# Performance work log

Measured on AMD Instinct MI355X. Metric: run time of the kernel, lower is better.

The kernel has to match this reference:

```python
import jax, jax.numpy as jnp
import numpy as np

DIM = 1024
HEADS = 16
DIM_HEAD = 64
INNER = HEADS * DIM_HEAD  # 1024
SCALE = DIM_HEAD ** -0.5


def setup_inputs() -> dict:
    key = jax.random.key(0)
    k_x, k_qkv, k_out, k_g, k_b = jax.random.split(key, 5)
    x = jax.random.normal(k_x, (4, 2048, DIM), dtype=jnp.float32)
    # LayerNorm affine params (torch default: weight=1, bias=0; keep learnable-shaped)
    ln_gamma = jnp.ones((DIM,), dtype=jnp.float32)
    ln_beta = jnp.zeros((DIM,), dtype=jnp.float32)
    w_qkv = jax.random.normal(k_qkv, (DIM, 3 * INNER), dtype=jnp.float32) * (DIM ** -0.5)
    w_out = jax.random.normal(k_out, (INNER, DIM), dtype=jnp.float32) * (INNER ** -0.5)
    return {"x": x, "ln_gamma": ln_gamma, "ln_beta": ln_beta, "w_qkv": w_qkv, "w_out": w_out}


def reference(x, ln_gamma, ln_beta, w_qkv, w_out):
    # LayerNorm (eps matches torch default 1e-5)
    mu = jnp.mean(x, axis=-1, keepdims=True)
    var = jnp.mean(jnp.square(x - mu), axis=-1, keepdims=True)
    xn = (x - mu) * jax.lax.rsqrt(var + 1e-5) * ln_gamma + ln_beta

    qkv = xn @ w_qkv  # [b, n, 3*inner]
    q, k, v = jnp.split(qkv, 3, axis=-1)

    def to_heads(t):  # b n (h d) -> b h n d
        b, n, _ = t.shape
        return t.reshape(b, n, HEADS, DIM_HEAD).transpose(0, 2, 1, 3)

    q, k, v = to_heads(q), to_heads(k), to_heads(v)

    dots = jnp.einsum('bhid,bhjd->bhij', q, k) * SCALE  # [b,h,n,n]
    attn = jax.nn.softmax(dots, axis=-1)
    out = jnp.einsum('bhij,bhjd->bhid', attn, v)  # [b,h,n,d]

    b, h, n, d = out.shape
    out = out.transpose(0, 2, 1, 3).reshape(b, n, h * d)  # b h n d -> b n (h d)
    return out @ w_out
```

## Files before the change

kernel.cpp:

```cpp
#include <hip/hip_runtime.h>

#define DIM 1024
#define HEADS 16
#define DHEAD 64
#define SEQ 2048
#define BATCH 4
#define ROWS (BATCH*SEQ)
#define QK_COLS (3*DIM)
#define QSCALE 0.18033688011112042f

typedef __bf16 bf16x8 __attribute__((ext_vector_type(8)));
typedef __bf16 bf16x4 __attribute__((ext_vector_type(4)));
typedef short s16x4 __attribute__((ext_vector_type(4)));
typedef float f32x4 __attribute__((ext_vector_type(4)));
typedef unsigned short u16;
typedef unsigned int u32;

__device__ __forceinline__ u16 f2bf(float f) {
  u32 u = __float_as_uint(f);
  u = (u + 0x7fffu + ((u >> 16) & 1u)) >> 16;
  return (u16)u;
}

__device__ __forceinline__ void gld16(const void* g, void* s) {
  __builtin_amdgcn_global_load_lds((__attribute__((address_space(1))) void*)g,
                                   (__attribute__((address_space(3))) void*)s, 16, 0, 0);
}

__device__ __forceinline__ float fexp2(float x) {
#if defined(__HIP_DEVICE_COMPILE__)
  return __builtin_amdgcn_exp2f(x);
#else
  return x;
#endif
}

__device__ __forceinline__ s16x4 pack_bf16(f32x4 v) {
  bf16x4 b = __builtin_convertvector(v, bf16x4);
  union { bf16x4 b; s16x4 s; } u; u.b = b; return u.s;
}

__global__ __launch_bounds__(256) void prep_kernel(
    const float* __restrict__ x, const float* __restrict__ gam, const float* __restrict__ bet,
    u16* __restrict__ xn,
    const float* __restrict__ wqkv, u16* __restrict__ wqkvT,
    const float* __restrict__ wout, u16* __restrict__ woutT) {
  __shared__ float tile[32][33];
  int bid = blockIdx.x, tid = threadIdx.x;
  if (bid < ROWS) {
    int lane = tid & 63, w = tid >> 6;
    const float4 xv = *(const float4*)(x + (size_t)bid*DIM + tid*4);
    float s = xv.x + xv.y + xv.z + xv.w;
    float q = xv.x*xv.x + xv.y*xv.y + xv.z*xv.z + xv.w*xv.w;
    for (int off = 32; off > 0; off >>= 1) { s += __shfl_xor(s, off, 64); q += __shfl_xor(q, off, 64); }
    float* red = &tile[0][0];
    if (lane == 0) { red[w] = s; red[4+w] = q; }
    __syncthreads();
    s = red[0]+red[1]+red[2]+red[3];
    q = red[4]+red[5]+red[6]+red[7];
    float mean = s * (1.0f/DIM);
    float rstd = rsqrtf(q*(1.0f/DIM) - mean*mean + 1e-5f);
    float4 gv = *(const float4*)(gam + tid*4);
    float4 bv = *(const float4*)(bet + tid*4);
    ushort4 o;
    o.x = f2bf((xv.x-mean)*rstd*gv.x + bv.x);
    o.y = f2bf((xv.y-mean)*rstd*gv.y + bv.y);
    o.z = f2bf((xv.z-mean)*rstd*gv.z + bv.z);
    o.w = f2bf((xv.w-mean)*rstd*gv.w + bv.w);
    *(ushort4*)(xn + (size_t)bid*DIM + tid*4) = o;
  } else {
    const float* in; u16* out; int R, C, c0, r0;
    if (bid < ROWS + 3072) {
      int t = bid - ROWS;
      in = wqkv; out = wqkvT; R = DIM; C = QK_COLS;
      c0 = (t % 96) * 32; r0 = (t / 96) * 32;
    } else {
      int t = bid - ROWS - 3072;
      in = wout; out = woutT; R = DIM; C = DIM;
      c0 = (t & 31) * 32; r0 = (t >> 5) * 32;
    }
    int tx = tid & 31, ty = tid >> 5;
    for (int i = 0; i < 32; i += 8)
      tile[ty+i][tx] = in[(size_t)(r0+ty+i)*C + c0 + tx];
    __syncthreads();
    for (int i = 0; i < 32; i += 8)
      out[(size_t)(c0+ty+i)*R + r0 + tx] = f2bf(tile[tx][ty+i]);
  }
}

template<int NOUT, int EPI>
__global__ __launch_bounds__(256, 2) void gemm_bt(const u16* __restrict__ A, const u16* __restrict__ Bt,
                                                  void* __restrict__ Cv, u16* __restrict__ vT, int K) {
  __shared__ alignas(16) u16 smem[16384];
  int tid = threadIdx.x;
  int lane = tid & 63, w = tid >> 6;
  int l = lane & 15, quad = lane >> 4;
  int wm = (w & 1) * 64, wn = (w >> 1) * 64;
  int m0 = blockIdx.y * 128, n0 = blockIdx.x * 128;
  const u16* Ag = A + (size_t)m0 * K;
  const u16* Bg = Bt + (size_t)n0 * K;
  bool sw = (EPI == 1) || (n0 < 2048);
  f32x4 z = {0.f, 0.f, 0.f, 0.f};
  f32x4 acc[4][4];
  for (int i = 0; i < 4; ++i) for (int j = 0; j < 4; ++j) acc[i][j] = z;

  #pragma unroll
  for (int c = 0; c < 2; ++c) {
    int idx = c*256 + tid;
    int row = idx >> 2, col = (idx & 3) << 3;
    gld16(Ag + (size_t)row*K + col, smem + idx*8);
    gld16(Bg + (size_t)row*K + col, smem + 4096 + idx*8);
  }

  int NT = K >> 5;
  for (int kt = 0; kt < NT; ++kt) {
    __syncthreads();
    const u16* As = smem + (kt & 1)*8192;
    const u16* Bs = As + 4096;
    if (kt + 1 < NT) {
      u16* dst = (u16*)smem + ((kt+1) & 1)*8192;
      int ko = (kt+1)*32;
      #pragma unroll
      for (int c = 0; c < 2; ++c) {
        int idx = c*256 + tid;
        int row = idx >> 2, col = (idx & 3) << 3;
        gld16(Ag + (size_t)row*K + ko + col, dst + idx*8);
        gld16(Bg + (size_t)row*K + ko + col, dst + 4096 + idx*8);
      }
    }
    bf16x8 af[4], bfr[4];
    #pragma unroll
    for (int t = 0; t < 4; ++t) {
      af[t]  = *(const bf16x8*)(As + (wm + t*16 + l)*32 + quad*8);
      bfr[t] = *(const bf16x8*)(Bs + (wn + t*16 + l)*32 + quad*8);
    }
    if (sw) {
      #pragma unroll
      for (int i = 0; i < 4; ++i)
        #pragma unroll
        for (int j = 0; j < 4; ++j)
          acc[i][j] = __builtin_amdgcn_mfma_f32_16x16x32_bf16(bfr[i], af[j], acc[i][j], 0, 0, 0);
    } else {
      #pragma unroll
      for (int i = 0; i < 4; ++i)
        #pragma unroll
        for (int j = 0; j < 4; ++j)
          acc[i][j] = __builtin_amdgcn_mfma_f32_16x16x32_bf16(af[i], bfr[j], acc[i][j], 0, 0, 0);
    }
  }

  if (EPI == 0) {
    u16* C = (u16*)Cv;
    int region = n0 >> 10;
    if (region == 0) {
      for (int i = 0; i < 4; ++i)
        for (int j = 0; j < 4; ++j) {
          int nq = n0 + wn + i*16 + quad*4;
          int m  = m0 + wm + j*16 + l;
          f32x4 v = acc[i][j] * QSCALE;
          *(s16x4*)(C + (size_t)m*QK_COLS + nq) = pack_bf16(v);
        }
    } else if (region == 1) {
      for (int i = 0; i < 4; ++i)
        for (int j = 0; j < 4; ++j) {
          int nq = n0 + wn + i*16 + quad*4;
          int m  = m0 + wm + j*16 + l;
          int d  = nq & 63;
          int col = (nq & ~63) | ((((d >> 3) ^ (m & 7)) << 3) | (d & 7));
          *(s16x4*)(C + (size_t)m*QK_COLS + col) = pack_bf16(acc[i][j]);
        }
    } else {
      for (int i = 0; i < 4; ++i)
        for (int j = 0; j < 4; ++j) {
          int mrow = m0 + wm + i*16 + quad*4;
          int hd   = (n0 - 2048) + wn + j*16 + l;
          int h = hd >> 6, d = hd & 63;
          int bb = mrow >> 11, nloc = mrow & 2047;
          int jloc = nloc & 31;
          int hi = jloc >> 4;
          int u  = ((nloc >> 5) & 3) * 4 + ((jloc >> 2) & 3);
          int c16 = u ^ (d & 15);
          int p = (nloc & ~127) | (c16 << 3) | (hi << 2);
          *(s16x4*)(vT + ((size_t)(bb*16 + h)*DHEAD + d)*SEQ + p) = pack_bf16(acc[i][j]);
        }
    }
  } else {
    float* C = (float*)Cv;
    for (int i = 0; i < 4; ++i)
      for (int j = 0; j < 4; ++j) {
        int n = n0 + wn + i*16 + quad*4;
        int m = m0 + wm + j*16 + l;
        *(f32x4*)(C + (size_t)m*NOUT + n) = acc[i][j];
      }
  }
}

__global__ __launch_bounds__(256, 2) void attn_kernel(const u16* __restrict__ qkv,
    const u16* __restrict__ vT, u16* __restrict__ aout) {
  __shared__ alignas(16) u16 smem[32768];
  int tid = threadIdx.x;
  int lane = tid & 63, w = tid >> 6;
  int l = lane & 15, quad = lane >> 4;
  int bh = blockIdx.x, qt = blockIdx.y;
  int b = bh >> 4, h = bh & 15;
  int qrow0 = b*SEQ + qt*128;

  bf16x8 aq[2][2];
  #pragma unroll
  for (int mt = 0; mt < 2; ++mt)
    #pragma unroll
    for (int ks = 0; ks < 2; ++ks)
      aq[mt][ks] = *(const bf16x8*)(qkv + (size_t)(qrow0 + w*32 + mt*16 + l)*QK_COLS + h*DHEAD + ks*32 + quad*8);

  f32x4 z = {0.f,0.f,0.f,0.f};
  f32x4 o[4][2];
  #pragma unroll
  for (int dt = 0; dt < 4; ++dt) for (int mt = 0; mt < 2; ++mt) o[dt][mt] = z;
  f32x4 psum[2] = {z, z};

  const u16* kbase = qkv + (size_t)b*SEQ*QK_COLS + DIM + h*DHEAD;
  const u16* vbase = vT + (size_t)bh*DHEAD*SEQ;

  #pragma unroll
  for (int c = 0; c < 4; ++c) {
    int idx = c*256 + tid;
    gld16(kbase + (size_t)(idx >> 3)*QK_COLS + ((idx & 7) << 3), smem + idx*8);
    gld16(vbase + (size_t)(idx >> 4)*SEQ + ((idx & 15) << 3), smem + 8192 + idx*8);
  }

  for (int kt = 0; kt < 16; ++kt) {
    __syncthreads();
    const u16* Kt = smem + (kt & 1)*16384;
    const u16* Vt = Kt + 8192;
    if (kt < 15) {
      u16* dst = (u16*)smem + ((kt+1) & 1)*16384;
      int krow0 = (kt+1)*128;
      #pragma unroll
      for (int c = 0; c < 4; ++c) {
        int idx = c*256 + tid;
        gld16(kbase + (size_t)(krow0 + (idx >> 3))*QK_COLS + ((idx & 7) << 3), dst + idx*8);
        gld16(vbase + (size_t)(idx >> 4)*SEQ + krow0 + ((idx & 15) << 3), dst + 8192 + idx*8);
      }
    }

    s16x4 pb[2][8];
    #pragma unroll
    for (int mt = 0; mt < 2; ++mt) {
      f32x4 st[8];
      #pragma unroll
      for (int jt = 0; jt < 8; ++jt) st[jt] = z;
      #pragma unroll
      for (int jt = 0; jt < 8; ++jt) {
        #pragma unroll
        for (int ks = 0; ks < 2; ++ks) {
          bf16x8 bk = *(const bf16x8*)(Kt + (jt*16 + l)*64 + (((ks*4 + quad) ^ (l & 7)) << 3));
          st[jt] = __builtin_amdgcn_mfma_f32_16x16x32_bf16(bk, aq[mt][ks], st[jt], 0,0,0);
        }
      }
      #pragma unroll
      for (int jt = 0; jt < 8; ++jt) {
        f32x4 p;
        p[0] = fexp2(st[jt][0]); p[1] = fexp2(st[jt][1]);
        p[2] = fexp2(st[jt][2]); p[3] = fexp2(st[jt][3]);
        psum[mt] += p;
        pb[mt][jt] = pack_bf16(p);
      }
    }

    #pragma unroll
    for (int jb = 0; jb < 4; ++jb) {
      union { s16x4 h[2]; bf16x8 v; } p0, p1;
      p0.h[0] = pb[0][2*jb]; p0.h[1] = pb[0][2*jb+1];
      p1.h[0] = pb[1][2*jb]; p1.h[1] = pb[1][2*jb+1];
      #pragma unroll
      for (int dt = 0; dt < 4; ++dt) {
        int d = dt*16 + l;
        bf16x8 av = *(const bf16x8*)(Vt + d*128 + (((jb*4 + quad) ^ l) << 3));
        o[dt][0] = __builtin_amdgcn_mfma_f32_16x16x32_bf16(av, p0.v, o[dt][0], 0,0,0);
        o[dt][1] = __builtin_amdgcn_mfma_f32_16x16x32_bf16(av, p1.v, o[dt][1], 0,0,0);
      }
    }
  }

  float li[2];
  #pragma unroll
  for (int mt = 0; mt < 2; ++mt) {
    float ps = psum[mt][0] + psum[mt][1] + psum[mt][2] + psum[mt][3];
    ps += __shfl_xor(ps, 16, 64);
    ps += __shfl_xor(ps, 32, 64);
    li[mt] = ps;
  }

  __syncthreads();
  u16* Ep = smem + w*2304;
  #pragma unroll
  for (int mt = 0; mt < 2; ++mt) {
    float inv = 1.0f / li[mt];
    #pragma unroll
    for (int dt = 0; dt < 4; ++dt)
      #pragma unroll
      for (int r = 0; r < 4; ++r)
        Ep[(mt*16 + l)*72 + dt*16 + quad*4 + r] = f2bf(o[dt][mt][r] * inv);
  }
  __asm__ volatile("s_waitcnt lgkmcnt(0)" ::: "memory");
  int lr = lane >> 1, half = lane & 1;
  size_t grow = (size_t)qrow0 + w*32 + lr;
  #pragma unroll
  for (int k = 0; k < 4; ++k) {
    uint4 vv = *(const uint4*)(Ep + lr*72 + half*32 + k*8);
    *(uint4*)(aout + grow*DIM + h*DHEAD + half*32 + k*8) = vv;
  }
}

extern "C" void kernel_launch(void* const* d_in, const int* in_sizes, int n_in,
                              void* d_out, int out_size, void* d_ws, size_t ws_size,
                              hipStream_t stream) {
  const float* x    = (const float*)d_in[0];
  const float* gam  = (const float*)d_in[1];
  const float* bet  = (const float*)d_in[2];
  const float* wqkv = (const float*)d_in[3];
  const float* wout = (const float*)d_in[4];
  float* out = (float*)d_out;

  u16* xn    = (u16*)d_ws;
  u16* wqkvT = xn    + (size_t)ROWS*DIM;
  u16* woutT = wqkvT + (size_t)QK_COLS*DIM;
  u16* qkvb  = woutT + (size_t)DIM*DIM;
  u16* vTb   = qkvb  + (size_t)ROWS*QK_COLS;
  u16* aoutb = vTb   + (size_t)64*DHEAD*SEQ;

  prep_kernel<<<ROWS + 3072 + 1024, 256, 0, stream>>>(x, gam, bet, xn, wqkv, wqkvT, wout, woutT);
  gemm_bt<QK_COLS,0><<<dim3(QK_COLS/128, ROWS/128), 256, 0, stream>>>(xn, wqkvT, (void*)qkvb, vTb, DIM);
  attn_kernel<<<dim3(64, SEQ/128), 256, 0, stream>>>(qkvb, vTb, aoutb);
  gemm_bt<DIM,1><<<dim3(DIM/128, ROWS/128), 256, 0, stream>>>(aoutb, woutT, (void*)out, nullptr, DIM);
}
```

Before: 271.6 us.

## Replace 128x128 GEMM with 256x256 tiled, phase-pipelined GEMM using XCD-aware block remap

Replaces the 128x128, 256-thread GEMM with a 256x256-tile, 512-thread kernel used by both the QKV and output projections. The new kernel stages A and B in a multi-buffered 128KB LDS schedule split into eight phases, each with explicit barriers, s_setprio around the MFMA bursts and manual vmcnt waits. It also remaps block IDs across the 8 XCDs to improve L2 locality. Larger tiles raise arithmetic intensity and cut global reloads. In exchange, only 128 blocks cover the output projection, which can leave most CUs idle, and the LDS footprint limits occupancy to one block per CU.

```diff
diff --git a/kernel.cpp b/kernel.cpp
--- a/kernel.cpp
+++ b/kernel.cpp
@@ -88,92 +88,124 @@
   }
 }
 
-template<int NOUT, int EPI>
-__global__ __launch_bounds__(256, 2) void gemm_bt(const u16* __restrict__ A, const u16* __restrict__ Bt,
-                                                  void* __restrict__ Cv, u16* __restrict__ vT, int K) {
-  __shared__ alignas(16) u16 smem[16384];
+template<int EPI>
+__global__ __launch_bounds__(512, 2) void gemm256(const u16* __restrict__ A, const u16* __restrict__ Bt,
+                                                  void* __restrict__ Cv, u16* __restrict__ vT,
+                                                  int K, int NBN, int NOUT) {
+  __shared__ alignas(16) u16 smem[65536];
   int tid = threadIdx.x;
   int lane = tid & 63, w = tid >> 6;
   int l = lane & 15, quad = lane >> 4;
-  int wm = (w & 1) * 64, wn = (w >> 1) * 64;
-  int m0 = blockIdx.y * 128, n0 = blockIdx.x * 128;
+  int wr = w >> 2, wc = w & 3;
+  int nwg = gridDim.x;
+  int qq8 = nwg >> 3;
+  int wg = (blockIdx.x & 7) * qq8 + (blockIdx.x >> 3);
+  int bm = wg / NBN, bn = wg % NBN;
+  int m0 = bm * 256, n0 = bn * 256;
   const u16* Ag = A + (size_t)m0 * K;
   const u16* Bg = Bt + (size_t)n0 * K;
   bool sw = (EPI == 1) || (n0 < 2048);
   f32x4 z = {0.f, 0.f, 0.f, 0.f};
-  f32x4 acc[4][4];
-  for (int i = 0; i < 4; ++i) for (int j = 0; j < 4; ++j) acc[i][j] = z;
-
-  #pragma unroll
-  for (int c = 0; c < 2; ++c) {
-    int idx = c*256 + tid;
-    int row = idx >> 2, col = (idx & 3) << 3;
-    gld16(Ag + (size_t)row*K + col, smem + idx*8);
-    gld16(Bg + (size_t)row*K + col, smem + 4096 + idx*8);
-  }
-
-  int NT = K >> 5;
-  for (int kt = 0; kt < NT; ++kt) {
-    __syncthreads();
-    const u16* As = smem + (kt & 1)*8192;
-    const u16* Bs = As + 4096;
-    if (kt + 1 < NT) {
-      u16* dst = (u16*)smem + ((kt+1) & 1)*8192;
-      int ko = (kt+1)*32;
-      #pragma unroll
-      for (int c = 0; c < 2; ++c) {
-        int idx = c*256 + tid;
-        int row = idx >> 2, col = (idx & 3) << 3;
-        gld16(Ag + (size_t)row*K + ko + col, dst + idx*8);
-        gld16(Bg + (size_t)row*K + ko + col, dst + 4096 + idx*8);
-      }
-    }
-    bf16x8 af[4], bfr[4];
-    #pragma unroll
-    for (int t = 0; t < 4; ++t) {
-      af[t]  = *(const bf16x8*)(As + (wm + t*16 + l)*32 + quad*8);
-      bfr[t] = *(const bf16x8*)(Bs + (wn + t*16 + l)*32 + quad*8);
-    }
-    if (sw) {
-      #pragma unroll
-      for (int i = 0; i < 4; ++i)
-        #pragma unroll
-        for (int j = 0; j < 4; ++j)
-          acc[i][j] = __builtin_amdgcn_mfma_f32_16x16x32_bf16(bfr[i], af[j], acc[i][j], 0, 0, 0);
-    } else {
-      #pragma unroll
-      for (int i = 0; i < 4; ++i)
-        #pragma unroll
-        for (int j = 0; j < 4; ++j)
-          acc[i][j] = __builtin_amdgcn_mfma_f32_16x16x32_bf16(af[i], bfr[j], acc[i][j], 0, 0, 0);
-    }
+  f32x4 acc[32];
+  #pragma unroll
+  for (int i = 0; i < 32; ++i) acc[i] = z;
+
+  #define AOFF(d, ks) ((d)*32768 + (ks)*8192)
+  #define BOFF(d, ks) ((d)*32768 + 16384 + (ks)*8192)
+  #define STG(dstOff, srcG, kofs) do { \
+    _Pragma("unroll") \
+    for (int c_ = 0; c_ < 2; ++c_) { \
+      int ch_ = c_*512 + tid; \
+      gld16((srcG) + (size_t)(ch_ >> 2)*K + (kofs) + ((ch_ & 3) << 3), \
+            smem + (dstOff) + ch_*8); \
+    } } while (0)
+
+  #define PHASE(d, h, ks, STAGE, VMN) do { \
+    const u16* Ar_ = smem + AOFF(d, ks); \
+    const u16* Br_ = smem + BOFF(d, ks); \
+    bf16x8 af_[4], bf_[4]; \
+    _Pragma("unroll") \
+    for (int mi = 0; mi < 4; ++mi) \
+      af_[mi] = *(const bf16x8*)(Ar_ + (wr*128 + (h)*64 + mi*16 + l)*32 + quad*8); \
+    _Pragma("unroll") \
+    for (int ni = 0; ni < 4; ++ni) \
+      bf_[ni] = *(const bf16x8*)(Br_ + (wc*64 + ni*16 + l)*32 + quad*8); \
+    STAGE; \
+    __builtin_amdgcn_s_barrier(); \
+    __builtin_amdgcn_s_setprio(1); \
+    if (sw) { \
+      _Pragma("unroll") \
+      for (int ni = 0; ni < 4; ++ni) \
+        _Pragma("unroll") \
+        for (int mi = 0; mi < 4; ++mi) \
+          acc[ni*8 + (h)*4 + mi] = __builtin_amdgcn_mfma_f32_16x16x32_bf16(bf_[ni], af_[mi], acc[ni*8 + (h)*4 + mi], 0, 0, 0); \
+    } else { \
+      _Pragma("unroll") \
+      for (int mi = 0; mi < 4; ++mi) \
+        _Pragma("unroll") \
+        for (int ni = 0; ni < 4; ++ni) \
+          acc[((h)*4 + mi)*4 + ni] = __builtin_amdgcn_mfma_f32_16x16x32_bf16(af_[mi], bf_[ni], acc[((h)*4 + mi)*4 + ni], 0, 0, 0); \
+    } \
+    __builtin_amdgcn_s_setprio(0); \
+    VMN; \
+    __builtin_amdgcn_s_barrier(); \
+  } while (0)
+
+  STG(AOFF(0,0), Ag, 0);  STG(BOFF(0,0), Bg, 0);
+  STG(AOFF(0,1), Ag, 32); STG(BOFF(0,1), Bg, 32);
+  STG(AOFF(1,0), Ag, 64); STG(BOFF(1,0), Bg, 64);
+  __asm__ volatile("s_waitcnt vmcnt(4)" ::: "memory");
+  __builtin_amdgcn_s_barrier();
+
+  int NT2 = K >> 7;
+  for (int t = 0; t < NT2; ++t) {
+    bool nl = (t < NT2 - 1);
+    int k1 = (2*t + 1) * 64, k2 = (2*t + 2) * 64, k3 = (2*t + 3) * 64;
+    PHASE(0,0,0, { STG(AOFF(1,1), Ag, k1+32); }, {});
+    PHASE(0,1,0, { STG(BOFF(1,1), Bg, k1+32); }, {});
+    PHASE(0,0,1, { if (nl) STG(AOFF(0,0), Ag, k2); }, {});
+    PHASE(0,1,1, { if (nl) STG(BOFF(0,0), Bg, k2); },
+          { if (nl) __asm__ volatile("s_waitcnt vmcnt(4)" ::: "memory");
+            else    __asm__ volatile("s_waitcnt vmcnt(0)" ::: "memory"); });
+    PHASE(1,0,0, { if (nl) STG(AOFF(0,1), Ag, k2+32); }, {});
+    PHASE(1,1,0, { if (nl) STG(BOFF(0,1), Bg, k2+32); }, {});
+    PHASE(1,0,1, { if (nl) STG(AOFF(1,0), Ag, k3); }, {});
+    PHASE(1,1,1, { if (nl) STG(BOFF(1,0), Bg, k3); },
+          { if (nl) __asm__ volatile("s_waitcnt vmcnt(4)" ::: "memory");
+            else    __asm__ volatile("s_waitcnt vmcnt(0)" ::: "memory"); });
   }
 
   if (EPI == 0) {
     u16* C = (u16*)Cv;
     int region = n0 >> 10;
     if (region == 0) {
-      for (int i = 0; i < 4; ++i)
-        for (int j = 0; j < 4; ++j) {
-          int nq = n0 + wn + i*16 + quad*4;
-          int m  = m0 + wm + j*16 + l;
-          f32x4 v = acc[i][j] * QSCALE;
-          *(s16x4*)(C + (size_t)m*QK_COLS + nq) = pack_bf16(v);
+      #pragma unroll
+      for (int ni = 0; ni < 4; ++ni)
+        #pragma unroll
+        for (int mi = 0; mi < 8; ++mi) {
+          int n = n0 + wc*64 + ni*16 + quad*4;
+          int m = m0 + wr*128 + mi*16 + l;
+          f32x4 v = acc[ni*8 + mi] * QSCALE;
+          *(s16x4*)(C + (size_t)m*QK_COLS + n) = pack_bf16(v);
         }
     } else if (region == 1) {
-      for (int i = 0; i < 4; ++i)
-        for (int j = 0; j < 4; ++j) {
-          int nq = n0 + wn + i*16 + quad*4;
-          int m  = m0 + wm + j*16 + l;
+      #pragma unroll
+      for (int ni = 0; ni < 4; ++ni)
+        #pragma unroll
+        for (int mi = 0; mi < 8; ++mi) {
+          int nq = n0 + wc*64 + ni*16 + quad*4;
+          int m  = m0 + wr*128 + mi*16 + l;
           int d  = nq & 63;
           int col = (nq & ~63) | ((((d >> 3) ^ (m & 7)) << 3) | (d & 7));
-          *(s16x4*)(C + (size_t)m*QK_COLS + col) = pack_bf16(acc[i][j]);
+          *(s16x4*)(C + (size_t)m*QK_COLS + col) = pack_bf16(acc[ni*8 + mi]);
         }
     } else {
-      for (int i = 0; i < 4; ++i)
-        for (int j = 0; j < 4; ++j) {
-          int mrow = m0 + wm + i*16 + quad*4;
-          int hd   = (n0 - 2048) + wn + j*16 + l;
+      #pragma unroll
+      for (int mi = 0; mi < 8; ++mi)
+        #pragma unroll
+        for (int ni = 0; ni < 4; ++ni) {
+          int mrow = m0 + wr*128 + mi*16 + quad*4;
+          int hd   = (n0 - 2048) + wc*64 + ni*16 + l;
           int h = hd >> 6, d = hd & 63;
           int bb = mrow >> 11, nloc = mrow & 2047;
           int jloc = nloc & 31;
@@ -181,18 +213,24 @@
           int u  = ((nloc >> 5) & 3) * 4 + ((jloc >> 2) & 3);
           int c16 = u ^ (d & 15);
           int p = (nloc & ~127) | (c16 << 3) | (hi << 2);
-          *(s16x4*)(vT + ((size_t)(bb*16 + h)*DHEAD + d)*SEQ + p) = pack_bf16(acc[i][j]);
+          *(s16x4*)(vT + ((size_t)(bb*16 + h)*DHEAD + d)*SEQ + p) = pack_bf16(acc[mi*4 + ni]);
         }
     }
   } else {
     float* C = (float*)Cv;
-    for (int i = 0; i < 4; ++i)
-      for (int j = 0; j < 4; ++j) {
-        int n = n0 + wn + i*16 + quad*4;
-        int m = m0 + wm + j*16 + l;
-        *(f32x4*)(C + (size_t)m*NOUT + n) = acc[i][j];
-      }
-  }
+    #pragma unroll
+    for (int ni = 0; ni < 4; ++ni)
+      #pragma unroll
+      for (int mi = 0; mi < 8; ++mi) {
+        int n = n0 + wc*64 + ni*16 + quad*4;
+        int m = m0 + wr*128 + mi*16 + l;
+        *(f32x4*)(C + (size_t)m*NOUT + n) = acc[ni*8 + mi];
+      }
+  }
+  #undef PHASE
+  #undef STG
+  #undef AOFF
+  #undef BOFF
 }
 
 __global__ __launch_bounds__(256, 2) void attn_kernel(const u16* __restrict__ qkv,
@@ -330,7 +368,7 @@
   u16* aoutb = vTb   + (size_t)64*DHEAD*SEQ;
 
   prep_kernel<<<ROWS + 3072 + 1024, 256, 0, stream>>>(x, gam, bet, xn, wqkv, wqkvT, wout, woutT);
-  gemm_bt<QK_COLS,0><<<dim3(QK_COLS/128, ROWS/128), 256, 0, stream>>>(xn, wqkvT, (void*)qkvb, vTb, DIM);
+  gemm256<0><<<(ROWS/256)*(QK_COLS/256), 512, 0, stream>>>(xn, wqkvT, (void*)qkvb, vTb, DIM, QK_COLS/256, 0);
   attn_kernel<<<dim3(64, SEQ/128), 256, 0, stream>>>(qkvb, vTb, aoutb);
-  gemm_bt<DIM,1><<<dim3(DIM/128, ROWS/128), 256, 0, stream>>>(aoutb, woutT, (void*)out, nullptr, DIM);
-}
+  gemm256<1><<<(ROWS/256)*(DIM/256), 512, 0, stream>>>(aoutb, woutT, (void*)out, nullptr, DIM, DIM/256, DIM);
+}
```

New measurement: 315.0 us. 16.0% more time.
